# Kernel tuning notes

Hardware: AMD Instinct MI355X
Metric: run time of the kernel (lower is better)

The kernel has to match this reference:

```python
import jax, jax.numpy as jnp
import numpy as np

EPS = 1e-8

def rms_norm(x, g):
    xf = x.astype(jnp.float32)
    ms = jnp.mean(xf * xf, axis=-1, keepdims=True)
    return (g * (xf * jax.lax.rsqrt(ms + EPS))).astype(x.dtype)

def setup_inputs() -> dict:
    key = jax.random.key(0)
    ks = jax.random.split(key, 10)
    B, S, D, H = 2, 2048, 1024, 16
    x = jax.random.normal(ks[0], (B, S, D), dtype=jnp.float32)
    p_bias = jax.random.normal(ks[1], (H, S, S), dtype=jnp.float32) * 0.02
    # additive causal mask [S, S]
    causal = jnp.tril(jnp.ones((S, S), dtype=bool))
    mask = jnp.where(causal, 0.0, -1e9).astype(jnp.float32)
    sd = 1.0 / np.sqrt(D)
    w_qkv = jax.random.normal(ks[2], (3 * D, D), dtype=jnp.float32) * sd
    w_u = jax.random.normal(ks[3], (D, D), dtype=jnp.float32) * sd
    g_ams = jnp.ones((D,), dtype=jnp.float32)
    w0 = jax.random.normal(ks[4], (D, D), dtype=jnp.float32) * sd
    w1 = jax.random.normal(ks[5], (2 * D, D), dtype=jnp.float32) * sd
    w3 = jax.random.normal(ks[6], (D, D), dtype=jnp.float32) * sd
    g_mffn = jnp.ones((D,), dtype=jnp.float32)
    return {"x": x, "p_bias": p_bias, "mask": mask, "w_qkv": w_qkv,
            "w_u": w_u, "g_ams": g_ams, "w0": w0, "w1": w1, "w3": w3,
            "g_mffn": g_mffn}

def reference(x, p_bias, mask, w_qkv, w_u, g_ams, w0, w1, w3, g_mffn):
    B, S, D = x.shape
    H = p_bias.shape[0]
    Dh = D // H
    scale = Dh ** -0.5
    # ---- AMS layer ----
    xn = rms_norm(x, g_ams)
    qkv = (xn @ w_qkv.T).reshape(B, S, 3, H, Dh)
    q, k, v = qkv[:, :, 0], qkv[:, :, 1], qkv[:, :, 2]  # [B,S,H,Dh]
    # scores: [B,H,S,S]
    score = jnp.einsum('bqhd,bkhd->bhqk', q, k) * scale
    score = score + p_bias[None] + mask[None, None]
    prob = jax.nn.silu(score)
    attn = jnp.einsum('bhqk,bkhd->bqhd', prob, v).reshape(B, S, D)
    u = jax.nn.silu(xn @ w_u.T)
    ams_out = attn * u
    # ---- MFFN layer ----
    o = ams_out @ w0.T + x
    on = rms_norm(o, g_mffn)
    x12 = on @ w1.T
    x1, x2 = jnp.split(x12, 2, axis=-1)
    hidden = jax.nn.silu(x1) * x2
    return hidden @ w3.T + o
```

## Files before the change

kernel.cpp:

```cpp
#include <hip/hip_runtime.h>
#include <hip/hip_bf16.h>
#include <cstdint>
#include <cstddef>

typedef __bf16 bf16x8 __attribute__((ext_vector_type(8)));
typedef float  f32x4  __attribute__((ext_vector_type(4)));
using u16 = unsigned short;
using u32 = unsigned int;

__device__ __forceinline__ float b2f(u16 u) {
  u32 v = ((u32)u) << 16;
  float f; __builtin_memcpy(&f, &v, 4); return f;
}
__device__ __forceinline__ u16 f2b(float f) {
  u32 v; __builtin_memcpy(&v, &f, 4);
  u32 r = v + 0x7fffu + ((v >> 16) & 1u);
  return (u16)(r >> 16);
}
__device__ __forceinline__ float silu(float x) {
  return x / (1.f + __expf(-x));
}
__device__ __forceinline__ f32x4 zero4() { f32x4 v = {0.f,0.f,0.f,0.f}; return v; }

typedef __attribute__((address_space(1))) const void* gas_ptr;
typedef __attribute__((address_space(3))) void*       las_ptr;
__device__ __forceinline__ void async_copy16(const void* g, void* l) {
  __builtin_amdgcn_global_load_lds((gas_ptr)g, (las_ptr)l, 16, 0, 0);
}

__global__ __launch_bounds__(256) void cvt_kernel(
    const float* __restrict__ wqkv, const float* __restrict__ wu,
    const float* __restrict__ w0,   const float* __restrict__ w1,
    const float* __restrict__ w3,
    u16* bqkv, u16* bu, u16* b0, u16* b1, u16* b3)
{
  const int blk = blockIdx.x;
  const float* src; u16* dst; int base;
  if      (blk < 3072) { src = wqkv; dst = bqkv; base = blk; }
  else if (blk < 4096) { src = wu;   dst = bu;   base = blk - 3072; }
  else if (blk < 5120) { src = w0;   dst = b0;   base = blk - 4096; }
  else if (blk < 7168) { src = w1;   dst = b1;   base = blk - 5120; }
  else                 { src = w3;   dst = b3;   base = blk - 7168; }
  const size_t i = (size_t)base * 1024 + threadIdx.x * 4;
  float4 v = *(const float4*)(src + i);
  uint2 o;
  o.x = (u32)f2b(v.x) | ((u32)f2b(v.y) << 16);
  o.y = (u32)f2b(v.z) | ((u32)f2b(v.w) << 16);
  *(uint2*)(dst + i) = o;
}

template<int EPI>
__global__ __launch_bounds__(256) void gemm_bt(
    const u16* __restrict__ A, const u16* __restrict__ Bw,
    const float* __restrict__ res, void* __restrict__ Cp,
    int M, int N, int K)
{
  __shared__ u16 sA[128 * 32];
  __shared__ u16 sB[128 * 32];

  const int t    = threadIdx.x;
  const int wave = t >> 6, lane = t & 63;
  const int quad = lane >> 4, l16 = lane & 15;
  const int wm = wave >> 1, wn = wave & 1;
  const int m0 = blockIdx.y * 128, n0 = blockIdx.x * 128;

  const int arow = t >> 2, achunk = t & 3;
  const u16* gA = A  + (size_t)(m0 + arow) * K + achunk * 8;
  const u16* gB = Bw + (size_t)(n0 + arow) * K + achunk * 8;
  u16* lA = sA + t * 8;
  u16* lB = sB + t * 8;

  f32x4 acc[4][4];
#pragma unroll
  for (int i = 0; i < 4; i++)
#pragma unroll
    for (int j = 0; j < 4; j++) acc[i][j] = zero4();

  for (int kb = 0; kb < K; kb += 32) {
    async_copy16(gA + kb,                 lA);
    async_copy16(gA + kb + (size_t)64*K,  lA + 2048);
    async_copy16(gB + kb,                 lB);
    async_copy16(gB + kb + (size_t)64*K,  lB + 2048);
    __syncthreads();

    bf16x8 af[4], bfr[4];
#pragma unroll
    for (int mi = 0; mi < 4; mi++)
      af[mi]  = *(const bf16x8*)(sA + (wm*64 + mi*16 + l16)*32 + quad*8);
#pragma unroll
    for (int ni = 0; ni < 4; ni++)
      bfr[ni] = *(const bf16x8*)(sB + (wn*64 + ni*16 + l16)*32 + quad*8);
#pragma unroll
    for (int mi = 0; mi < 4; mi++)
#pragma unroll
      for (int ni = 0; ni < 4; ni++)
        acc[mi][ni] = __builtin_amdgcn_mfma_f32_16x16x32_bf16(af[mi], bfr[ni], acc[mi][ni], 0, 0, 0);
    __syncthreads();
  }

#pragma unroll
  for (int mi = 0; mi < 4; mi++) {
#pragma unroll
    for (int ni = 0; ni < 4; ni++) {
#pragma unroll
      for (int r = 0; r < 4; r++) {
        const int row = m0 + wm*64 + mi*16 + quad*4 + r;
        const int col = n0 + wn*64 + ni*16 + l16;
        const size_t idx = (size_t)row * N + col;
        float v = acc[mi][ni][r];
        if constexpr (EPI == 0) {
          ((u16*)Cp)[idx] = f2b(v);
        } else if constexpr (EPI == 1) {
          ((u16*)Cp)[idx] = f2b(silu(v));
        } else {
          ((float*)Cp)[idx] = v + res[idx];
        }
      }
    }
  }
}

__global__ __launch_bounds__(256) void vtrans_kernel(
    const u16* __restrict__ qkv, u16* __restrict__ vt)
{
  __shared__ u16 tile[64][72];
  const int st = blockIdx.x, bh = blockIdx.y;
  const int b = bh >> 4, h = bh & 15;
  const int t = threadIdx.x;
#pragma unroll
  for (int i = 0; i < 2; i++) {
    const int c = i * 256 + t;
    const int row = c >> 3, cc = c & 7;
    uint4 v = *(const uint4*)(qkv + (size_t)(b*2048 + st*64 + row)*3072 + 2048 + h*64 + cc*8);
    *(uint4*)(&tile[row][cc*8]) = v;
  }
  __syncthreads();
#pragma unroll
  for (int i = 0; i < 2; i++) {
    const int c = i * 256 + t;
    const int dh = c >> 3, cc = c & 7;
    u16 tmp[8];
#pragma unroll
    for (int j = 0; j < 8; j++) tmp[j] = tile[cc*8 + j][dh];
    *(uint4*)(vt + ((size_t)bh*64 + dh)*2048 + st*64 + cc*8) = *(uint4*)tmp;
  }
}

__global__ __launch_bounds__(1024) void attn_kernel(
    const u16* __restrict__ qkv,
    const u16* __restrict__ vt,
    const float* __restrict__ p_bias,
    u16* __restrict__ attn_out)
{
  constexpr int S = 2048, D3 = 3072;
  __shared__ u16 sQ [128 * 64];
  __shared__ u16 sK [128 * 64];
  __shared__ u16 sVt[ 64 * 128];
  __shared__ u16 sP [128 * 128];

  const int t    = threadIdx.x;
  const int wave = t >> 6, lane = t & 63;
  const int quad = lane >> 4, l16 = lane & 15;
  const int p  = blockIdx.x & 7, bh = blockIdx.x >> 3;
  const int b  = bh >> 4, h = bh & 15;
  const int wsq = wave & 3, wsk = wave >> 2;
  const int wpq = wave & 3, wpd = wave >> 2;
  const float scale = 0.125f;

  const int srow8 = lane >> 3, sc8 = lane & 7;
  const int srow16 = lane >> 4, sc16 = lane & 15;

#pragma unroll 1
  for (int sel = 0; sel < 2; sel++) {
    const int qt = sel ? 15 - p : p;
    const int q0 = qt * 128;

    __syncthreads();
    {
      const int row = wave * 8 + srow8;
      const int gc  = sc8 ^ (row & 7);
      async_copy16(qkv + (size_t)(b*S + q0 + row)*D3 + h*64 + gc*8,
                   sQ + wave*512 + lane*8);
    }

    f32x4 oacc[2];
    oacc[0] = zero4(); oacc[1] = zero4();

    for (int kt = 0; kt <= qt; kt++) {
      const int k0 = kt * 128;
      __syncthreads();
      {
        const int row = wave * 8 + srow8;
        const int gc  = sc8 ^ (row & 7);
        async_copy16(qkv + (size_t)(b*S + k0 + row)*D3 + 1024 + h*64 + gc*8,
                     sK + wave*512 + lane*8);
        const int vrow = wave * 4 + srow16;
        const int vgc  = sc16 ^ (vrow & 15);
        async_copy16(vt + ((size_t)bh*64 + vrow)*2048 + k0 + vgc*8,
                     sVt + wave*512 + lane*8);
      }
      __syncthreads();

      float bias[2][2][4];
#pragma unroll
      for (int mi = 0; mi < 2; mi++)
#pragma unroll
        for (int ni = 0; ni < 2; ni++)
#pragma unroll
          for (int r = 0; r < 4; r++) {
            const int q = wsq*32 + mi*16 + quad*4 + r;
            const int k = wsk*32 + ni*16 + l16;
            bias[mi][ni][r] = p_bias[((size_t)h*S + q0 + q)*S + k0 + k];
          }

      bf16x8 aq[2][2], bk[2][2];
#pragma unroll
      for (int mi = 0; mi < 2; mi++)
#pragma unroll
        for (int kk = 0; kk < 2; kk++) {
          const int row = wsq*32 + mi*16 + l16;
          const int phys = (quad + kk*4) ^ (row & 7);
          aq[mi][kk] = *(const bf16x8*)(sQ + row*64 + phys*8);
        }
#pragma unroll
      for (int ni = 0; ni < 2; ni++)
#pragma unroll
        for (int kk = 0; kk < 2; kk++) {
          const int row = wsk*32 + ni*16 + l16;
          const int phys = (quad + kk*4) ^ (row & 7);
          bk[ni][kk] = *(const bf16x8*)(sK + row*64 + phys*8);
        }

      f32x4 sacc[2][2];
#pragma unroll
      for (int mi = 0; mi < 2; mi++)
#pragma unroll
        for (int ni = 0; ni < 2; ni++) {
          f32x4 s = zero4();
          s = __builtin_amdgcn_mfma_f32_16x16x32_bf16(aq[mi][0], bk[ni][0], s, 0, 0, 0);
          s = __builtin_amdgcn_mfma_f32_16x16x32_bf16(aq[mi][1], bk[ni][1], s, 0, 0, 0);
          sacc[mi][ni] = s;
        }

#pragma unroll
      for (int mi = 0; mi < 2; mi++)
#pragma unroll
        for (int ni = 0; ni < 2; ni++)
#pragma unroll
          for (int r = 0; r < 4; r++) {
            const int q = wsq*32 + mi*16 + quad*4 + r;
            const int k = wsk*32 + ni*16 + l16;
            const int qi = q0 + q, ki = k0 + k;
            float v = sacc[mi][ni][r] * scale + bias[mi][ni][r];
            v = (ki <= qi) ? silu(v) : 0.f;
            const int pc = (k >> 3) ^ (q & 15);
            sP[q*128 + pc*8 + (k & 7)] = f2b(v);
          }
      __syncthreads();

#pragma unroll
      for (int kk = 0; kk < 4; kk++) {
        bf16x8 ap[2], bv;
#pragma unroll
        for (int mi = 0; mi < 2; mi++) {
          const int row = wpq*32 + mi*16 + l16;
          const int phys = (quad + kk*4) ^ (row & 15);
          ap[mi] = *(const bf16x8*)(sP + row*128 + phys*8);
        }
        {
          const int row = wpd*16 + l16;
          const int phys = (quad + kk*4) ^ (row & 15);
          bv = *(const bf16x8*)(sVt + row*128 + phys*8);
        }
#pragma unroll
        for (int mi = 0; mi < 2; mi++)
          oacc[mi] = __builtin_amdgcn_mfma_f32_16x16x32_bf16(ap[mi], bv, oacc[mi], 0, 0, 0);
      }
    }

#pragma unroll
    for (int mi = 0; mi < 2; mi++)
#pragma unroll
      for (int r = 0; r < 4; r++) {
        const int q  = wpq*32 + mi*16 + quad*4 + r;
        const int dh = wpd*16 + l16;
        attn_out[(size_t)(b*S + q0 + q)*1024 + h*64 + dh] = f2b(oacc[mi][r]);
      }
  }
}

__global__ __launch_bounds__(256) void rmsnorm_kernel(
    const float* __restrict__ x, const float* __restrict__ g, u16* __restrict__ out)
{
  const int row = blockIdx.x, t = threadIdx.x;
  const int wave = t >> 6, lane = t & 63;
  const size_t base = (size_t)row * 1024;
  float v[4];
#pragma unroll
  for (int i = 0; i < 4; i++) v[i] = x[base + i * 256 + t];
  float ss = v[0]*v[0] + v[1]*v[1] + v[2]*v[2] + v[3]*v[3];
#pragma unroll
  for (int off = 32; off; off >>= 1) ss += __shfl_down(ss, off);
  __shared__ float red[4];
  if (lane == 0) red[wave] = ss;
  __syncthreads();
  const float r = rsqrtf((red[0] + red[1] + red[2] + red[3]) * (1.f / 1024.f) + 1e-8f);
#pragma unroll
  for (int i = 0; i < 4; i++) {
    const int j = i * 256 + t;
    out[base + j] = f2b(g[j] * v[i] * r);
  }
}

__global__ __launch_bounds__(256) void mul_kernel(
    const u16* __restrict__ a, const u16* __restrict__ b, u16* __restrict__ o, int n)
{
  const int i = (blockIdx.x * 256 + threadIdx.x) * 8;
  if (i >= n) return;
  uint4 av = *(const uint4*)(a + i), bv = *(const uint4*)(b + i);
  const u16* pa = (const u16*)&av; const u16* pb = (const u16*)&bv;
  uint4 ov; u16* po = (u16*)&ov;
#pragma unroll
  for (int j = 0; j < 8; j++) po[j] = f2b(b2f(pa[j]) * b2f(pb[j]));
  *(uint4*)(o + i) = ov;
}

__global__ __launch_bounds__(256) void glu_kernel(
    const u16* __restrict__ x12, u16* __restrict__ hid)
{
  const int idx = blockIdx.x * 256 + threadIdx.x;
  const int row = idx >> 7, cc = idx & 127;
  const u16* p1 = x12 + (size_t)row * 2048 + cc * 8;
  uint4 v1 = *(const uint4*)p1, v2 = *(const uint4*)(p1 + 1024);
  const u16* a = (const u16*)&v1; const u16* b = (const u16*)&v2;
  uint4 ov; u16* po = (u16*)&ov;
#pragma unroll
  for (int j = 0; j < 8; j++) po[j] = f2b(silu(b2f(a[j])) * b2f(b[j]));
  *(uint4*)(hid + (size_t)row * 1024 + cc * 8) = ov;
}

extern "C" void kernel_launch(void* const* d_in, const int* in_sizes, int n_in,
                              void* d_out, int out_size, void* d_ws, size_t ws_size,
                              hipStream_t stream)
{
  const float* x      = (const float*)d_in[0];
  const float* pbias  = (const float*)d_in[1];
  const float* w_qkv  = (const float*)d_in[3];
  const float* w_u    = (const float*)d_in[4];
  const float* g_ams  = (const float*)d_in[5];
  const float* w0     = (const float*)d_in[6];
  const float* w1     = (const float*)d_in[7];
  const float* w3     = (const float*)d_in[8];
  const float* g_mffn = (const float*)d_in[9];

  constexpr int M = 4096, D = 1024;
  char* ws = (char*)d_ws;
  u16*   xn    = (u16*)ws;
  u16*   qkv   = (u16*)(ws + (8u  << 20));
  u16*   ubuf  = (u16*)(ws + (32u << 20));
  u16*   attn  = (u16*)(ws + (40u << 20));
  float* obuf  = (float*)(ws + (48u << 20));
  u16*   vt    = (u16*)(ws + (48u << 20));
  u16*   bqkv  = (u16*)(ws + (64u << 20));
  u16*   bu    = (u16*)(ws + (70u << 20));
  u16*   b0    = (u16*)(ws + (72u << 20));
  u16*   b1    = (u16*)(ws + (74u << 20));
  u16*   b3    = (u16*)(ws + (78u << 20));

  cvt_kernel<<<8192, 256, 0, stream>>>(w_qkv, w_u, w0, w1, w3, bqkv, bu, b0, b1, b3);
  rmsnorm_kernel<<<M, 256, 0, stream>>>(x, g_ams, xn);
  gemm_bt<0><<<dim3(24, 32), 256, 0, stream>>>(xn, bqkv, nullptr, qkv, M, 3072, D);
  gemm_bt<1><<<dim3(8, 32), 256, 0, stream>>>(xn, bu, nullptr, ubuf, M, D, D);
  vtrans_kernel<<<dim3(32, 32), 256, 0, stream>>>(qkv, vt);
  attn_kernel<<<256, 1024, 0, stream>>>(qkv, vt, pbias, attn);
  mul_kernel<<<2048, 256, 0, stream>>>(attn, ubuf, xn, M * D);
  gemm_bt<2><<<dim3(8, 32), 256, 0, stream>>>(xn, b0, x, obuf, M, D, D);
  rmsnorm_kernel<<<M, 256, 0, stream>>>(obuf, g_mffn, ubuf);
  gemm_bt<0><<<dim3(16, 32), 256, 0, stream>>>(ubuf, b1, nullptr, qkv, M, 2048, D);
  glu_kernel<<<2048, 256, 0, stream>>>(qkv, attn);
  gemm_bt<3><<<dim3(8, 32), 256, 0, stream>>>(attn, b3, obuf, (float*)d_out, M, D, D);
}
```

Measured before the change: 631.4 us.

## Fuse elementwise ops into GEMM/attention epilogues, add 128x64 tiles and grid swizzle

Removes the separate mul and GLU kernels by multiplying the u gate inside the attention epilogue and computing silu(x1)*x2 inside a new dual-accumulator GEMM. The N=1024 GEMMs move to 128x64 tiles, doubling the workgroup count to 512 to fill the CUs better. All GEMMs also get an XCD-aware block index remap meant to improve L2 locality. This saves several full-tensor round trips to HBM and two launches, at the cost of lower per-block reuse in the smaller tiles.

```diff
diff --git a/kernel.cpp b/kernel.cpp
--- a/kernel.cpp
+++ b/kernel.cpp
@@ -62,7 +62,12 @@
   const int wave = t >> 6, lane = t & 63;
   const int quad = lane >> 4, l16 = lane & 15;
   const int wm = wave >> 1, wn = wave & 1;
-  const int m0 = blockIdx.y * 128, n0 = blockIdx.x * 128;
+
+  const int nwg = gridDim.x * gridDim.y;
+  const int bid = blockIdx.y * gridDim.x + blockIdx.x;
+  const int v   = (bid & 7) * (nwg >> 3) + (bid >> 3);
+  const int bx  = v % gridDim.x, by = v / gridDim.x;
+  const int m0 = by * 128, n0 = bx * 128;
 
   const int arow = t >> 2, achunk = t & 3;
   const u16* gA = A  + (size_t)(m0 + arow) * K + achunk * 8;
@@ -107,14 +112,159 @@
         const int row = m0 + wm*64 + mi*16 + quad*4 + r;
         const int col = n0 + wn*64 + ni*16 + l16;
         const size_t idx = (size_t)row * N + col;
-        float v = acc[mi][ni][r];
+        float vv = acc[mi][ni][r];
         if constexpr (EPI == 0) {
-          ((u16*)Cp)[idx] = f2b(v);
+          ((u16*)Cp)[idx] = f2b(vv);
         } else if constexpr (EPI == 1) {
-          ((u16*)Cp)[idx] = f2b(silu(v));
+          ((u16*)Cp)[idx] = f2b(silu(vv));
         } else {
-          ((float*)Cp)[idx] = v + res[idx];
-        }
+          ((float*)Cp)[idx] = vv + res[idx];
+        }
+      }
+    }
+  }
+}
+
+template<int EPI>
+__global__ __launch_bounds__(256) void gemm64_bt(
+    const u16* __restrict__ A, const u16* __restrict__ Bw,
+    const float* __restrict__ res, void* __restrict__ Cp,
+    int M, int N, int K)
+{
+  __shared__ u16 sA[128 * 32];
+  __shared__ u16 sB[ 64 * 32];
+
+  const int t    = threadIdx.x;
+  const int wave = t >> 6, lane = t & 63;
+  const int quad = lane >> 4, l16 = lane & 15;
+  const int wm = wave >> 1, wn = wave & 1;
+
+  const int nwg = gridDim.x * gridDim.y;
+  const int bid = blockIdx.y * gridDim.x + blockIdx.x;
+  const int v   = (bid & 7) * (nwg >> 3) + (bid >> 3);
+  const int bx  = v & (gridDim.x - 1), by = v / gridDim.x;
+  const int m0 = by * 128, n0 = bx * 64;
+
+  const int arow = t >> 2, achunk = t & 3;
+  const u16* gA = A  + (size_t)(m0 + arow) * K + achunk * 8;
+  const u16* gB = Bw + (size_t)(n0 + arow) * K + achunk * 8;
+  u16* lA = sA + t * 8;
+  u16* lB = sB + t * 8;
+
+  f32x4 acc[4][2];
+#pragma unroll
+  for (int i = 0; i < 4; i++) { acc[i][0] = zero4(); acc[i][1] = zero4(); }
+
+  for (int kb = 0; kb < K; kb += 32) {
+    async_copy16(gA + kb,                 lA);
+    async_copy16(gA + kb + (size_t)64*K,  lA + 2048);
+    async_copy16(gB + kb,                 lB);
+    __syncthreads();
+
+    bf16x8 af[4], bfr[2];
+#pragma unroll
+    for (int mi = 0; mi < 4; mi++)
+      af[mi]  = *(const bf16x8*)(sA + (wm*64 + mi*16 + l16)*32 + quad*8);
+#pragma unroll
+    for (int ni = 0; ni < 2; ni++)
+      bfr[ni] = *(const bf16x8*)(sB + (wn*32 + ni*16 + l16)*32 + quad*8);
+#pragma unroll
+    for (int mi = 0; mi < 4; mi++)
+#pragma unroll
+      for (int ni = 0; ni < 2; ni++)
+        acc[mi][ni] = __builtin_amdgcn_mfma_f32_16x16x32_bf16(af[mi], bfr[ni], acc[mi][ni], 0, 0, 0);
+    __syncthreads();
+  }
+
+#pragma unroll
+  for (int mi = 0; mi < 4; mi++) {
+#pragma unroll
+    for (int ni = 0; ni < 2; ni++) {
+#pragma unroll
+      for (int r = 0; r < 4; r++) {
+        const int row = m0 + wm*64 + mi*16 + quad*4 + r;
+        const int col = n0 + wn*32 + ni*16 + l16;
+        const size_t idx = (size_t)row * N + col;
+        float vv = acc[mi][ni][r];
+        if constexpr (EPI == 1) {
+          ((u16*)Cp)[idx] = f2b(silu(vv));
+        } else {
+          ((float*)Cp)[idx] = vv + res[idx];
+        }
+      }
+    }
+  }
+}
+
+__global__ __launch_bounds__(256) void gemm_glu(
+    const u16* __restrict__ A, const u16* __restrict__ Bw,
+    u16* __restrict__ hid, int K)
+{
+  __shared__ u16 sA [128 * 32];
+  __shared__ u16 sB1[ 64 * 32];
+  __shared__ u16 sB2[ 64 * 32];
+
+  const int t    = threadIdx.x;
+  const int wave = t >> 6, lane = t & 63;
+  const int quad = lane >> 4, l16 = lane & 15;
+  const int wm = wave >> 1, wn = wave & 1;
+
+  const int nwg = gridDim.x * gridDim.y;
+  const int bid = blockIdx.y * gridDim.x + blockIdx.x;
+  const int v   = (bid & 7) * (nwg >> 3) + (bid >> 3);
+  const int bx  = v & (gridDim.x - 1), by = v / gridDim.x;
+  const int m0 = by * 128, n0 = bx * 64;
+
+  const int arow = t >> 2, achunk = t & 3;
+  const u16* gA  = A  + (size_t)(m0 + arow) * K + achunk * 8;
+  const u16* gB1 = Bw + (size_t)(n0 + arow) * K + achunk * 8;
+  const u16* gB2 = Bw + (size_t)(n0 + 1024 + arow) * K + achunk * 8;
+  u16* lA  = sA  + t * 8;
+  u16* lB1 = sB1 + t * 8;
+  u16* lB2 = sB2 + t * 8;
+
+  f32x4 acc1[4][2], acc2[4][2];
+#pragma unroll
+  for (int i = 0; i < 4; i++) {
+    acc1[i][0] = zero4(); acc1[i][1] = zero4();
+    acc2[i][0] = zero4(); acc2[i][1] = zero4();
+  }
+
+  for (int kb = 0; kb < K; kb += 32) {
+    async_copy16(gA + kb,                 lA);
+    async_copy16(gA + kb + (size_t)64*K,  lA + 2048);
+    async_copy16(gB1 + kb,                lB1);
+    async_copy16(gB2 + kb,                lB2);
+    __syncthreads();
+
+    bf16x8 af[4], b1f[2], b2f[2];
+#pragma unroll
+    for (int mi = 0; mi < 4; mi++)
+      af[mi] = *(const bf16x8*)(sA + (wm*64 + mi*16 + l16)*32 + quad*8);
+#pragma unroll
+    for (int ni = 0; ni < 2; ni++) {
+      b1f[ni] = *(const bf16x8*)(sB1 + (wn*32 + ni*16 + l16)*32 + quad*8);
+      b2f[ni] = *(const bf16x8*)(sB2 + (wn*32 + ni*16 + l16)*32 + quad*8);
+    }
+#pragma unroll
+    for (int mi = 0; mi < 4; mi++)
+#pragma unroll
+      for (int ni = 0; ni < 2; ni++) {
+        acc1[mi][ni] = __builtin_amdgcn_mfma_f32_16x16x32_bf16(af[mi], b1f[ni], acc1[mi][ni], 0, 0, 0);
+        acc2[mi][ni] = __builtin_amdgcn_mfma_f32_16x16x32_bf16(af[mi], b2f[ni], acc2[mi][ni], 0, 0, 0);
+      }
+    __syncthreads();
+  }
+
+#pragma unroll
+  for (int mi = 0; mi < 4; mi++) {
+#pragma unroll
+    for (int ni = 0; ni < 2; ni++) {
+#pragma unroll
+      for (int r = 0; r < 4; r++) {
+        const int row = m0 + wm*64 + mi*16 + quad*4 + r;
+        const int col = n0 + wn*32 + ni*16 + l16;
+        hid[(size_t)row * 1024 + col] = f2b(silu(acc1[mi][ni][r]) * acc2[mi][ni][r]);
       }
     }
   }
@@ -150,7 +300,8 @@
     const u16* __restrict__ qkv,
     const u16* __restrict__ vt,
     const float* __restrict__ p_bias,
-    u16* __restrict__ attn_out)
+    const u16* __restrict__ ub,
+    u16* __restrict__ am_out)
 {
   constexpr int S = 2048, D3 = 3072;
   __shared__ u16 sQ [128 * 64];
@@ -251,10 +402,10 @@
             const int q = wsq*32 + mi*16 + quad*4 + r;
             const int k = wsk*32 + ni*16 + l16;
             const int qi = q0 + q, ki = k0 + k;
-            float v = sacc[mi][ni][r] * scale + bias[mi][ni][r];
-            v = (ki <= qi) ? silu(v) : 0.f;
+            float vv = sacc[mi][ni][r] * scale + bias[mi][ni][r];
+            vv = (ki <= qi) ? silu(vv) : 0.f;
             const int pc = (k >> 3) ^ (q & 15);
-            sP[q*128 + pc*8 + (k & 7)] = f2b(v);
+            sP[q*128 + pc*8 + (k & 7)] = f2b(vv);
           }
       __syncthreads();
 
@@ -284,7 +435,8 @@
       for (int r = 0; r < 4; r++) {
         const int q  = wpq*32 + mi*16 + quad*4 + r;
         const int dh = wpd*16 + l16;
-        attn_out[(size_t)(b*S + q0 + q)*1024 + h*64 + dh] = f2b(oacc[mi][r]);
+        const size_t oidx = (size_t)(b*S + q0 + q)*1024 + h*64 + dh;
+        am_out[oidx] = f2b(oacc[mi][r] * b2f(ub[oidx]));
       }
   }
 }
@@ -310,33 +462,6 @@
     const int j = i * 256 + t;
     out[base + j] = f2b(g[j] * v[i] * r);
   }
-}
-
-__global__ __launch_bounds__(256) void mul_kernel(
-    const u16* __restrict__ a, const u16* __restrict__ b, u16* __restrict__ o, int n)
-{
-  const int i = (blockIdx.x * 256 + threadIdx.x) * 8;
-  if (i >= n) return;
-  uint4 av = *(const uint4*)(a + i), bv = *(const uint4*)(b + i);
-  const u16* pa = (const u16*)&av; const u16* pb = (const u16*)&bv;
-  uint4 ov; u16* po = (u16*)&ov;
-#pragma unroll
-  for (int j = 0; j < 8; j++) po[j] = f2b(b2f(pa[j]) * b2f(pb[j]));
-  *(uint4*)(o + i) = ov;
-}
-
-__global__ __launch_bounds__(256) void glu_kernel(
-    const u16* __restrict__ x12, u16* __restrict__ hid)
-{
-  const int idx = blockIdx.x * 256 + threadIdx.x;
-  const int row = idx >> 7, cc = idx & 127;
-  const u16* p1 = x12 + (size_t)row * 2048 + cc * 8;
-  uint4 v1 = *(const uint4*)p1, v2 = *(const uint4*)(p1 + 1024);
-  const u16* a = (const u16*)&v1; const u16* b = (const u16*)&v2;
-  uint4 ov; u16* po = (u16*)&ov;
-#pragma unroll
-  for (int j = 0; j < 8; j++) po[j] = f2b(silu(b2f(a[j])) * b2f(b[j]));
-  *(uint4*)(hid + (size_t)row * 1024 + cc * 8) = ov;
 }
 
 extern "C" void kernel_launch(void* const* d_in, const int* in_sizes, int n_in,
@@ -358,7 +483,7 @@
   u16*   xn    = (u16*)ws;
   u16*   qkv   = (u16*)(ws + (8u  << 20));
   u16*   ubuf  = (u16*)(ws + (32u << 20));
-  u16*   attn  = (u16*)(ws + (40u << 20));
+  u16*   am    = (u16*)(ws + (40u << 20));
   float* obuf  = (float*)(ws + (48u << 20));
   u16*   vt    = (u16*)(ws + (48u << 20));
   u16*   bqkv  = (u16*)(ws + (64u << 20));
@@ -370,13 +495,11 @@
   cvt_kernel<<<8192, 256, 0, stream>>>(w_qkv, w_u, w0, w1, w3, bqkv, bu, b0, b1, b3);
   rmsnorm_kernel<<<M, 256, 0, stream>>>(x, g_ams, xn);
   gemm_bt<0><<<dim3(24, 32), 256, 0, stream>>>(xn, bqkv, nullptr, qkv, M, 3072, D);
-  gemm_bt<1><<<dim3(8, 32), 256, 0, stream>>>(xn, bu, nullptr, ubuf, M, D, D);
+  gemm64_bt<1><<<dim3(16, 32), 256, 0, stream>>>(xn, bu, nullptr, ubuf, M, D, D);
   vtrans_kernel<<<dim3(32, 32), 256, 0, stream>>>(qkv, vt);
-  attn_kernel<<<256, 1024, 0, stream>>>(qkv, vt, pbias, attn);
-  mul_kernel<<<2048, 256, 0, stream>>>(attn, ubuf, xn, M * D);
-  gemm_bt<2><<<dim3(8, 32), 256, 0, stream>>>(xn, b0, x, obuf, M, D, D);
+  attn_kernel<<<256, 1024, 0, stream>>>(qkv, vt, pbias, ubuf, am);
+  gemm64_bt<2><<<dim3(16, 32), 256, 0, stream>>>(am, b0, x, obuf, M, D, D);
   rmsnorm_kernel<<<M, 256, 0, stream>>>(obuf, g_mffn, ubuf);
-  gemm_bt<0><<<dim3(16, 32), 256, 0, stream>>>(ubuf, b1, nullptr, qkv, M, 2048, D);
-  glu_kernel<<<2048, 256, 0, stream>>>(qkv, attn);
-  gemm_bt<3><<<dim3(8, 32), 256, 0, stream>>>(attn, b3, obuf, (float*)d_out, M, D, D);
-}
+  gemm_glu<<<dim3(16, 32), 256, 0, stream>>>(ubuf, b1, am, D);
+  gemm64_bt<3><<<dim3(16, 32), 256, 0, stream>>>(am, b3, obuf, (float*)d_out, M, D, D);
+}
```

Measured after the change: 601.9 us. 4.7% less time.
